# Optimization experiments

Hardware: AMD Instinct MI355X
Metric: run time of the kernel (lower is better)

The kernel has to match this reference:

```python
import jax, jax.numpy as jnp
import numpy as np
import math

NUM_ITER = 5
FEAT_STRIDE = 16
GAUSS_SIGMA = 1.0
HINGE_THRESHOLD = -999.0
MIN_FILTER_REG = 1e-3
ALPHA_EPS = 0.0


def apply_filter(feat, weights):
    # feat: (ni, ns, C, H, W); weights: (ns, C, fH, fW) -> scores (ni, ns, oH, oW)
    ni, ns, C, H, W = feat.shape
    fH, fW = weights.shape[-2], weights.shape[-1]
    x = feat.reshape(ni, ns * C, H, W)
    out = jax.lax.conv_general_dilated(
        x, weights, window_strides=(1, 1),
        padding=((fH // 2, fH // 2), (fW // 2, fW // 2)),
        dimension_numbers=('NCHW', 'OIHW', 'NCHW'),
        feature_group_count=ns)
    return out  # (ni, ns, oH, oW); oH = H + (fH+1)%2


def get_label(center, out_sz, sigma):
    # center: (ni, ns, 2) in (row, col) order
    k0 = jnp.arange(out_sz[0], dtype=jnp.float32)[None, None, :, None]
    k1 = jnp.arange(out_sz[1], dtype=jnp.float32)[None, None, None, :]
    g0 = jnp.exp(-0.5 / (sigma * sigma) * (k0 - center[..., 0][..., None, None]) ** 2)
    g1 = jnp.exp(-0.5 / (sigma * sigma) * (k1 - center[..., 1][..., None, None]) ** 2)
    return g0 * g1  # (ni, ns, oH, oW)


def _forward(weights, feat, bb, log_step_length, filter_reg):
    ni, ns = feat.shape[0], feat.shape[1]
    fH, fW = weights.shape[-2], weights.shape[-1]
    out_sz = (feat.shape[-2] + (fH + 1) % 2, feat.shape[-1] + (fW + 1) % 2)
    step = jnp.exp(log_step_length)[0]
    reg = jnp.maximum(filter_reg * filter_reg, MIN_FILTER_REG ** 2)[0]
    dmap_offset = jnp.array([fH % 2, fW % 2], jnp.float32) / 2.0
    # (x, y) -> (row, col), feature-grid coordinates
    center = ((bb[..., :2] + bb[..., 2:] / 2.0) / FEAT_STRIDE)[..., ::-1] - dmap_offset
    label = get_label(center, out_sz, GAUSS_SIGMA)
    mask = (label > HINGE_THRESHOLD).astype(feat.dtype)
    label = label * mask
    sw = math.sqrt(1.0 / ni)

    losses = []
    for _ in range(NUM_ITER):
        scores = apply_filter(feat, weights)
        scores_act = mask * scores + (1.0 - mask) * jax.nn.relu(scores)
        score_mask = mask + (1.0 - mask) * (jax.lax.stop_gradient(scores) > 0).astype(scores.dtype)
        residuals = sw * (scores_act - label)
        losses.append((jnp.sum(residuals ** 2) + reg * jnp.sum(weights ** 2)) / ns)
        residuals_mapped = score_mask * (sw * residuals)
        # feat-transpose = adjoint of apply_filter w.r.t. the filter weights
        _, vjp_fn = jax.vjp(lambda w: apply_filter(feat, w), weights)
        data_grad = vjp_fn(residuals_mapped)[0]
        weights_grad = data_grad + reg * weights
        scores_grad = apply_filter(feat, weights_grad)
        scores_grad = sw * (score_mask * scores_grad)
        alpha_num = jnp.sum(weights_grad ** 2, axis=(1, 2, 3))  # (ns,)
        alpha_den = jnp.maximum(
            jnp.sum(scores_grad.reshape(ni, ns, -1) ** 2, axis=(0, 2))
            + (reg + ALPHA_EPS) * alpha_num, 1e-8)
        alpha = alpha_num / alpha_den
        weights = weights - step * alpha[:, None, None, None] * weights_grad

    scores = apply_filter(feat, weights)
    scores = mask * scores + (1.0 - mask) * jax.nn.relu(scores)
    losses.append((jnp.sum((sw * (scores - label)) ** 2) + reg * jnp.sum(weights ** 2)) / ns)
    return weights, jnp.stack(losses)


def setup_inputs() -> dict:
    key = jax.random.key(0)
    k1, k2, k3, k4 = jax.random.split(key, 4)
    ni, ns, C, H, W, fH, fW = 3, 32, 512, 22, 22, 4, 4
    weights = 0.01 * jax.random.normal(k1, (ns, C, fH, fW), jnp.float32)
    feat = jax.random.normal(k2, (ni, ns, C, H, W), jnp.float32)
    # boxes (x, y, w, h) in image coords (image size = 22*16 = 352)
    xy = jax.random.uniform(k3, (ni, ns, 2), jnp.float32, 50.0, 250.0)
    wh = jax.random.uniform(k4, (ni, ns, 2), jnp.float32, 32.0, 96.0)
    bb = jnp.concatenate([xy, wh], axis=-1)
    log_step_length = jnp.zeros((1,), jnp.float32)  # log(1.0)
    filter_reg = 0.01 * jnp.ones((1,), jnp.float32)
    return {"weights": weights, "feat": feat, "bb": bb,
            "log_step_length": log_step_length, "filter_reg": filter_reg}


def reference(weights, feat, bb, log_step_length, filter_reg):
    return _forward(weights, feat, bb, log_step_length, filter_reg)
```

## Files before the change

kernel.cpp:

```cpp
#include <hip/hip_runtime.h>
#include <hip/hip_fp16.h>

#define NI 3
#define NS 32
#define CHN 512
#define OH 23
#define P2 529
#define NP 50784
#define UV 484
#define WSZ 262144
#define KTOT 1536
#define RSP 1544

typedef unsigned int uint32;
typedef unsigned short u16;
typedef _Float16 h2 __attribute__((ext_vector_type(2)));
typedef _Float16 f16x8 __attribute__((ext_vector_type(8)));
typedef float f32x4 __attribute__((ext_vector_type(4)));

#define OFF_FEATT 0UL
#define OFF_LABEL 47579136UL
#define OFF_S0    47782272UL
#define OFF_S1    47985408UL
#define OFF_SGRAW 48188544UL
#define OFF_WG    48391680UL
#define OFF_WGF16 49440256UL
#define OFF_W0F16 49964544UL
#define OFF_PART  50488832UL
#define OFF_FEATC 50521600UL
#define OFF_S0B   100853248UL
#define OFF_SGB   101056384UL

#define P_DEN   0
#define P_NUM   4320
#define P_LOSS  5600
#define P_WSQ0  5760
#define P_WSQA  5792
#define P_WSQ5  6816
#define P_L5    7840

__device__ __forceinline__ float waveSum(float v) {
#pragma unroll
  for (int o = 32; o > 0; o >>= 1) v += __shfl_xor(v, o, 64);
  return v;
}

__global__ __launch_bounds__(256) void k_setup(const float* __restrict__ feat,
                                               const float* __restrict__ w0,
                                               const float* __restrict__ bb,
                                               u16* __restrict__ featT,
                                               u16* __restrict__ featC,
                                               u16* __restrict__ w0f16,
                                               float* __restrict__ wmaster,
                                               float* __restrict__ label,
                                               float* __restrict__ part) {
  __shared__ uint32 lds32[64 * 121];
  __shared__ float sred[4];
  int b = blockIdx.x, tid = threadIdx.x;
  if (b < 1536) {
    int snT = b >> 4, r4 = b & 15;
    int cb = r4 >> 1, uvh = r4 & 1;
    int s = snT / 3, n = snT % 3;
    const float* fsrc =
        feat + ((size_t)n * NS + s) * CHN * UV + (size_t)(cb * 64) * UV + uvh * 242;
#pragma unroll
    for (int it = 0; it < 31; ++it) {
      int idx = it * 256 + tid;
      if (idx < 7744) {
        int r = (unsigned)idx / 121u;
        int j = idx - r * 121;
        float2 v = *(const float2*)(fsrc + (size_t)r * UV + 2 * j);
        lds32[idx] = (uint32)__half_as_ushort(__float2half(v.x)) |
                     ((uint32)__half_as_ushort(__float2half(v.y)) << 16);
      }
    }
    __syncthreads();
    uint32* dstT = (uint32*)featT +
                   ((size_t)(snT * 4 + (cb >> 1)) * UV + uvh * 242) * 64 + (cb & 1) * 32;
#pragma unroll
    for (int it = 0; it < 16; ++it) {
      int o = it * 256 + tid;
      if (o < 3872) {
        int uv = o >> 4, kp = o & 15;
        int j = uv >> 1, sh = (uv & 1) * 16;
        uint32 a0 = lds32[(4 * kp + 0) * 121 + j];
        uint32 a1 = lds32[(4 * kp + 1) * 121 + j];
        uint32 a2 = lds32[(4 * kp + 2) * 121 + j];
        uint32 a3 = lds32[(4 * kp + 3) * 121 + j];
        uint2 val;
        val.x = ((a0 >> sh) & 0xffffu) | (((a1 >> sh) & 0xffffu) << 16);
        val.y = ((a2 >> sh) & 0xffffu) | (((a3 >> sh) & 0xffffu) << 16);
        *(uint2*)(dstT + (size_t)uv * 64 + 2 * kp) = val;
      }
    }
    uint32* dstC =
        (uint32*)featC + ((size_t)(s * CHN + cb * 64)) * 768 + n * 256 + uvh * 121;
    if (uvh == 0) {
#pragma unroll
      for (int it = 0; it < 31; ++it) {
        int idx = it * 256 + tid;
        if (idx < 7744) {
          int c = (unsigned)idx / 121u;
          int j = idx - c * 121;
          dstC[(size_t)c * 768 + j] = lds32[idx];
        }
      }
    } else {
#pragma unroll
      for (int it = 0; it < 34; ++it) {
        int idx = it * 256 + tid;
        if (idx < 8640) {
          int c = (unsigned)idx / 135u;
          int j = idx - c * 135;
          dstC[(size_t)c * 768 + j] = (j < 121) ? lds32[c * 121 + j] : 0u;
        }
      }
    }
  } else if (b < 1568) {
    int s = b - 1536;
    for (int i = tid; i < 8192; i += 256) {
      int tap = i >> 9, c = i & 511;
      w0f16[(size_t)s * 8192 + i] =
          __half_as_ushort(__float2half(w0[(size_t)s * 8192 + c * 16 + tap]));
    }
    float sq = 0.f;
    for (int i = tid; i < 8192; i += 256) {
      float v = w0[(size_t)s * 8192 + i];
      wmaster[(size_t)s * 8192 + i] = v;
      sq += v * v;
    }
    sq = waveSum(sq);
    if ((tid & 63) == 0) sred[tid >> 6] = sq;
    __syncthreads();
    if (tid == 0) part[P_WSQ0 + s] = sred[0] + sred[1] + sred[2] + sred[3];
  } else {
    int p = (b - 1568) * 256 + tid;
    if (p < NP) {
      int nsid = p / P2, rem = p % P2;
      int i = rem / OH, j = rem % OH;
      const float* bp = bb + (size_t)nsid * 4;
      float cr = (bp[1] + 0.5f * bp[3]) * 0.0625f;
      float cc = (bp[0] + 0.5f * bp[2]) * 0.0625f;
      float dy = (float)i - cr, dx = (float)j - cc;
      label[p] = __expf(-0.5f * (dy * dy + dx * dx));
    }
  }
}

__global__ __launch_bounds__(1024) void k_conv_fwd(const u16* __restrict__ featT,
                                                   const u16* __restrict__ wf16,
                                                   float* __restrict__ outA,
                                                   float* __restrict__ outB) {
  __shared__ uint32 w_lds[16 * 132];
  __shared__ float G[496 * 17];
  int tid = threadIdx.x;
  int bidx = blockIdx.x;
  int snT = bidx >> 1, ch = bidx & 1;
  int s = snT / 3, n = snT - s * 3;
  const uint32* wsrc = (const uint32*)(wf16 + (size_t)s * 8192) + ch * 128;
  for (int i = tid; i < 2048; i += 1024) {
    int tap = i >> 7, p = i & 127;
    w_lds[tap * 132 + p] = wsrc[(size_t)tap * 256 + p];
  }
  __syncthreads();
  int wave = tid >> 6, lane = tid & 63;
  int q = lane >> 4, m16 = lane & 15;
  int t0 = wave, t1 = wave + 16;
  bool has2 = (t1 < 31);
  f32x4 acc0 = {0.f, 0.f, 0.f, 0.f}, acc1 = {0.f, 0.f, 0.f, 0.f};
  size_t base = (size_t)snT * 4 * UV * 128;
  int r0i = t0 * 16 + m16;
  int r1i = has2 ? t1 * 16 + m16 : 483;
  if (r1i > 483) r1i = 483;
  size_t row0 = (size_t)r0i * 128;
  size_t row1 = (size_t)r1i * 128;
#pragma unroll
  for (int ks = 0; ks < 8; ++ks) {
    int cb = ch * 2 + (ks >> 2), cin = (ks & 3) * 32;
    size_t cbase = base + (size_t)cb * UV * 128 + cin + q * 8;
    f16x8 a0 = *(const f16x8*)(featT + cbase + row0);
    uint4 bw = *(const uint4*)&w_lds[m16 * 132 + ks * 16 + q * 4];
    f16x8 bf = __builtin_bit_cast(f16x8, bw);
    acc0 = __builtin_amdgcn_mfma_f32_16x16x32_f16(a0, bf, acc0, 0, 0, 0);
    if (has2) {
      f16x8 a1 = *(const f16x8*)(featT + cbase + row1);
      acc1 = __builtin_amdgcn_mfma_f32_16x16x32_f16(a1, bf, acc1, 0, 0, 0);
    }
  }
#pragma unroll
  for (int r = 0; r < 4; ++r) G[(t0 * 16 + q * 4 + r) * 17 + m16] = acc0[r];
  if (has2) {
#pragma unroll
    for (int r = 0; r < 4; ++r) G[(t1 * 16 + q * 4 + r) * 17 + m16] = acc1[r];
  }
  __syncthreads();
  if (tid < P2) {
    int y = tid / 23, x = tid - y * 23;
    float val = 0.f;
#pragma unroll
    for (int ky = 0; ky < 4; ++ky) {
      int u = y + ky - 2;
      if ((unsigned)u < 22u) {
#pragma unroll
        for (int kx = 0; kx < 4; ++kx) {
          int v = x + kx - 2;
          if ((unsigned)v < 22u) val += G[(u * 22 + v) * 17 + ky * 4 + kx];
        }
      }
    }
    float* dst = ch ? outB : outA;
    dst[(size_t)(n * NS + s) * P2 + tid] = val;
  }
}

__global__ __launch_bounds__(1024) void k_adjoint(
    int t, const u16* __restrict__ featC, const float* __restrict__ label,
    const float* __restrict__ s0a, const float* __restrict__ s0b,
    const float* __restrict__ scores_old, float* __restrict__ scores_new,
    const float* __restrict__ sga, const float* __restrict__ sgb,
    float* __restrict__ wg, u16* __restrict__ wgf16, float* __restrict__ wmaster,
    float* __restrict__ part, const float* __restrict__ lsl,
    const float* __restrict__ fr) {
  __shared__ float r_lds[3 * P2];
  __shared__ __align__(16) u16 rs[16 * RSP];
  __shared__ __align__(16) float kred[3 * 4 * 64 * 4];
  __shared__ float lred[16], nred[16], wred[16], dend[16];
  int tid = threadIdx.x;
  int s = blockIdx.x >> 3, chunk = blockIdx.x & 7;
  int c0 = chunk * 64;
  float step = __expf(lsl[0]);
  float frv = fr[0];
  float reg = fmaxf(frv * frv, 1e-6f);

  float alpha_p = 0.f;
  if (t >= 1) {
    const float* np_ = part + P_NUM + (size_t)((t - 1) * NS + s) * 8;
    float nu = 0.f;
#pragma unroll
    for (int i = 0; i < 8; ++i) nu += np_[i];
    float dp = 0.f;
    for (int pl = tid; pl < 1587; pl += 1024) {
      int nn = (unsigned)pl / (unsigned)P2;
      int rem = pl - nn * P2;
      size_t gp = (size_t)(nn * NS + s) * P2 + rem;
      float g = sga[gp] + sgb[gp];
      dp += g * g;
    }
    dp = waveSum(dp);
    if ((tid & 63) == 0) dend[tid >> 6] = dp;
    __syncthreads();
    float de = 0.f;
#pragma unroll
    for (int i = 0; i < 16; ++i) de += dend[i];
    alpha_p = nu / fmaxf(de * (1.0f / 3.0f) + reg * nu, 1e-8f);
  }

  float lsum = 0.f;
  for (int pl = tid; pl < 1587; pl += 1024) {
    int nn = (unsigned)pl / (unsigned)P2;
    int rem = pl - nn * P2;
    size_t gp = (size_t)(nn * NS + s) * P2 + rem;
    float S = (t <= 1) ? (s0a[gp] + s0b[gp]) : scores_old[gp];
    if (t >= 1) S -= step * alpha_p * (sga[gp] + sgb[gp]);
    float d = S - label[gp];
    r_lds[nn * P2 + rem] = d * (1.0f / 3.0f);
    if (chunk == 0) {
      if (t >= 1) scores_new[gp] = S;
      lsum += d * d;
    }
  }
  lsum = waveSum(lsum);
  if ((tid & 63) == 0) lred[tid >> 6] = lsum;
  __syncthreads();
  if (chunk == 0 && tid == 0) {
    float L = 0.f;
#pragma unroll
    for (int i = 0; i < 16; ++i) L += lred[i];
    part[P_LOSS + t * NS + s] = L * (1.0f / 3.0f);
  }

  for (int idx = tid; idx < 16 * RSP; idx += 1024) {
    int tap = (unsigned)idx / (unsigned)RSP;
    int k = idx - tap * RSP;
    float val = 0.f;
    if (k < KTOT) {
      int n = k >> 9, uv = k & 511;
      if (uv < UV) {
        int u = (unsigned)uv / 22u;
        int v = uv - u * 22;
        int ky = tap >> 2, kx = tap & 3;
        int y = u + 2 - ky, x = v + 2 - kx;
        if ((unsigned)y < 23u && (unsigned)x < 23u) val = r_lds[n * P2 + y * OH + x];
      }
    }
    rs[idx] = __half_as_ushort(__float2half(val));
  }
  __syncthreads();

  int wave = tid >> 6, lane = tid & 63;
  int q = lane >> 4, m16 = lane & 15;
  int tile = wave & 3, kq = wave >> 2;
  int c = c0 + tile * 16 + m16;
  const u16* arow = featC + ((size_t)(s * CHN + c)) * KTOT + kq * 384 + q * 8;
  const u16* brow = rs + m16 * RSP + kq * 384 + q * 8;
  f32x4 acc = {0.f, 0.f, 0.f, 0.f};
#pragma unroll
  for (int ks = 0; ks < 12; ++ks) {
    f16x8 a = *(const f16x8*)(arow + ks * 32);
    f16x8 bf = *(const f16x8*)(brow + ks * 32);
    acc = __builtin_amdgcn_mfma_f32_16x16x32_f16(a, bf, acc, 0, 0, 0);
  }
  if (kq) *(f32x4*)&kred[(((kq - 1) * 4 + tile) * 64 + lane) * 4] = acc;
  __syncthreads();

  float num_part = 0.f, wsq_part = 0.f;
  if (kq == 0) {
#pragma unroll
    for (int kk = 0; kk < 3; ++kk)
      acc += *(const f32x4*)&kred[((kk * 4 + tile) * 64 + lane) * 4];
    int tap = m16;
    int ccb = c0 + tile * 16 + q * 4;
    union { u16 h[4]; uint2 v2; } pk;
#pragma unroll
    for (int r = 0; r < 4; ++r) {
      int cc = ccb + r;
      size_t widx = (size_t)s * 8192 + (size_t)cc * 16 + tap;
      float wold = wmaster[widx];
      float wnew = wold;
      if (t >= 1) {
        wnew = wold - step * alpha_p * wg[widx];
        wmaster[widx] = wnew;
      }
      float wgn = acc[r] + reg * wnew;
      wg[widx] = wgn;
      pk.h[r] = __half_as_ushort(__float2half(wgn));
      wsq_part += wnew * wnew;
      num_part += wgn * wgn;
    }
    *(uint2*)&wgf16[(size_t)s * 8192 + (size_t)tap * 512 + ccb] = pk.v2;
  }
  num_part = waveSum(num_part);
  wsq_part = waveSum(wsq_part);
  if (lane == 0) {
    nred[wave] = num_part;
    wred[wave] = wsq_part;
  }
  __syncthreads();
  if (tid == 0) {
    float nsum = 0.f, wsum = 0.f;
#pragma unroll
    for (int i = 0; i < 16; ++i) {
      nsum += nred[i];
      wsum += wred[i];
    }
    part[P_NUM + (size_t)(t * NS + s) * 8 + chunk] = nsum;
    if (t >= 1) part[P_WSQA + (size_t)((t - 1) * NS + s) * 8 + chunk] = wsum;
  }
}

__global__ __launch_bounds__(1024) void k_den(const float* __restrict__ sga,
                                              const float* __restrict__ sgb,
                                              float* __restrict__ part) {
  __shared__ float dend[16];
  int s = blockIdx.x, tid = threadIdx.x;
  float dp = 0.f;
  for (int pl = tid; pl < 1587; pl += 1024) {
    int nn = (unsigned)pl / (unsigned)P2;
    int rem = pl - nn * P2;
    size_t gp = (size_t)(nn * NS + s) * P2 + rem;
    float g = sga[gp] + sgb[gp];
    dp += g * g;
  }
  dp = waveSum(dp);
  if ((tid & 63) == 0) dend[tid >> 6] = dp;
  __syncthreads();
  if (tid == 0) {
    float de = 0.f;
#pragma unroll
    for (int i = 0; i < 16; ++i) de += dend[i];
    part[P_DEN + s] = de * (1.0f / 3.0f);
  }
}

__device__ __forceinline__ float alphaFinal(const float* __restrict__ part, int s,
                                            float reg) {
  const float* np_ = part + P_NUM + (size_t)(4 * NS + s) * 8;
  float nu = 0.f;
#pragma unroll
  for (int i = 0; i < 8; ++i) nu += np_[i];
  float de = part[P_DEN + s];
  return nu / fmaxf(de + reg * nu, 1e-8f);
}

__global__ void k_final(float* __restrict__ wmaster, const float* __restrict__ wg,
                        const float* __restrict__ scores4, const float* __restrict__ sga,
                        const float* __restrict__ sgb, const float* __restrict__ label,
                        float* __restrict__ part, const float* __restrict__ lsl,
                        const float* __restrict__ fr) {
  __shared__ float alpha_s[32];
  __shared__ float red4[4];
  int b = blockIdx.x, tid = threadIdx.x;
  float step = __expf(lsl[0]);
  float frv = fr[0];
  float reg = fmaxf(frv * frv, 1e-6f);
  if (tid < 32) alpha_s[tid] = alphaFinal(part, tid, reg);
  __syncthreads();
  if (b < 1024) {
    int idx = b * 256 + tid;
    int s = idx >> 13;
    float w5 = wmaster[idx] - step * alpha_s[s] * wg[idx];
    wmaster[idx] = w5;
    float sq = waveSum(w5 * w5);
    if ((tid & 63) == 0) red4[tid >> 6] = sq;
    __syncthreads();
    if (tid == 0) part[P_WSQ5 + b] = red4[0] + red4[1] + red4[2] + red4[3];
  } else {
    int p = (b - 1024) * 256 + tid;
    float contrib = 0.f;
    if (p < NP) {
      int nsid = p / P2;
      int s = nsid & 31;
      float s5 = scores4[p] - step * alpha_s[s] * (sga[p] + sgb[p]);
      float d = s5 - label[p];
      contrib = d * d;
    }
    contrib = waveSum(contrib);
    if ((tid & 63) == 0) red4[tid >> 6] = contrib;
    __syncthreads();
    if (tid == 0)
      part[P_L5 + (b - 1024)] = (red4[0] + red4[1] + red4[2] + red4[3]) * (1.0f / 3.0f);
  }
}

__global__ void k_losses(float* __restrict__ out_losses, const float* __restrict__ part,
                         const float* __restrict__ fr) {
  __shared__ float red[8];
  int tid = threadIdx.x;
  float frv = fr[0];
  float reg = fmaxf(frv * frv, 1e-6f);
  float v5 = 0.f;
  for (int i = tid; i < 1024; i += 256) v5 += part[P_WSQ5 + i];
  v5 = waveSum(v5);
  if ((tid & 63) == 0) red[tid >> 6] = v5;
  __syncthreads();
  float wsq5 = red[0] + red[1] + red[2] + red[3];
  float l5 = 0.f;
  for (int i = tid; i < 199; i += 256) l5 += part[P_L5 + i];
  l5 = waveSum(l5);
  if ((tid & 63) == 0) red[4 + (tid >> 6)] = l5;
  __syncthreads();
  float loss5 = red[4] + red[5] + red[6] + red[7];
  if (tid < 5) {
    int t = tid;
    float ls = 0.f;
    for (int i = 0; i < 32; ++i) ls += part[P_LOSS + t * NS + i];
    float ws_ = 0.f;
    if (t == 0) {
      for (int i = 0; i < 32; ++i) ws_ += part[P_WSQ0 + i];
    } else {
      for (int i = 0; i < 256; ++i) ws_ += part[P_WSQA + (t - 1) * 256 + i];
    }
    out_losses[t] = (ls + reg * ws_) * (1.0f / 32.0f);
  }
  if (tid == 5) out_losses[5] = (loss5 + reg * wsq5) * (1.0f / 32.0f);
}

extern "C" void kernel_launch(void* const* d_in, const int* in_sizes, int n_in,
                              void* d_out, int out_size, void* d_ws, size_t ws_size,
                              hipStream_t stream) {
  const float* w0 = (const float*)d_in[0];
  const float* feat = (const float*)d_in[1];
  const float* bb = (const float*)d_in[2];
  const float* lsl = (const float*)d_in[3];
  const float* fr = (const float*)d_in[4];
  float* out = (float*)d_out;
  char* ws = (char*)d_ws;
  u16* featT = (u16*)(ws + OFF_FEATT);
  float* label = (float*)(ws + OFF_LABEL);
  float* s0 = (float*)(ws + OFF_S0);
  float* s0b = (float*)(ws + OFF_S0B);
  float* s1 = (float*)(ws + OFF_S1);
  float* sga = (float*)(ws + OFF_SGRAW);
  float* sgb = (float*)(ws + OFF_SGB);
  float* wg = (float*)(ws + OFF_WG);
  u16* wgf16 = (u16*)(ws + OFF_WGF16);
  u16* w0f16 = (u16*)(ws + OFF_W0F16);
  float* part = (float*)(ws + OFF_PART);
  u16* featC = (u16*)(ws + OFF_FEATC);

  k_setup<<<1767, 256, 0, stream>>>(feat, w0, bb, featT, featC, w0f16, out, label, part);
  k_conv_fwd<<<192, 1024, 0, stream>>>(featT, w0f16, s0, s0b);
  for (int t = 0; t < 5; ++t) {
    const float* so = (t <= 1) ? s0 : ((t & 1) ? s0 : s1);
    float* sn = (t & 1) ? s1 : s0;
    k_adjoint<<<256, 1024, 0, stream>>>(t, featC, label, s0, s0b, so, sn, sga, sgb, wg,
                                        wgf16, out, part, lsl, fr);
    k_conv_fwd<<<192, 1024, 0, stream>>>(featT, wgf16, sga, sgb);
  }
  k_den<<<32, 1024, 0, stream>>>(sga, sgb, part);
  k_final<<<1223, 256, 0, stream>>>(out, wg, s0, sga, sgb, label, part, lsl, fr);
  k_losses<<<1, 256, 0, stream>>>(out + WSZ, part, fr);
}
```

Before: 358.9 us.

## Build channel-major feature copy lazily inside first adjoint pass with k-blocked layout

Removes the featC transpose/write from the setup kernel. The first adjoint iteration now reads fp32 features directly, converts them to fp16, feeds them to the MFMA and writes them out in a new k-block-major layout. Later iterations read that layout with strided loads. This saves one pass over the features in setup and overlaps the conversion with compute, but the first adjoint becomes heavier and reads from global memory with less coalescing.

```diff
diff --git a/kernel.cpp b/kernel.cpp
--- a/kernel.cpp
+++ b/kernel.cpp
@@ -10,6 +10,7 @@
 #define UV 484
 #define WSZ 262144
 #define KTOT 1536
+#define NKB 48
 #define RSP 1544
 
 typedef unsigned int uint32;
@@ -49,7 +50,6 @@
                                                const float* __restrict__ w0,
                                                const float* __restrict__ bb,
                                                u16* __restrict__ featT,
-                                               u16* __restrict__ featC,
                                                u16* __restrict__ w0f16,
                                                float* __restrict__ wmaster,
                                                float* __restrict__ label,
@@ -93,29 +93,6 @@
         *(uint2*)(dstT + (size_t)uv * 64 + 2 * kp) = val;
       }
     }
-    uint32* dstC =
-        (uint32*)featC + ((size_t)(s * CHN + cb * 64)) * 768 + n * 256 + uvh * 121;
-    if (uvh == 0) {
-#pragma unroll
-      for (int it = 0; it < 31; ++it) {
-        int idx = it * 256 + tid;
-        if (idx < 7744) {
-          int c = (unsigned)idx / 121u;
-          int j = idx - c * 121;
-          dstC[(size_t)c * 768 + j] = lds32[idx];
-        }
-      }
-    } else {
-#pragma unroll
-      for (int it = 0; it < 34; ++it) {
-        int idx = it * 256 + tid;
-        if (idx < 8640) {
-          int c = (unsigned)idx / 135u;
-          int j = idx - c * 135;
-          dstC[(size_t)c * 768 + j] = (j < 121) ? lds32[c * 121 + j] : 0u;
-        }
-      }
-    }
   } else if (b < 1568) {
     int s = b - 1536;
     for (int i = tid; i < 8192; i += 256) {
@@ -214,12 +191,12 @@
 }
 
 __global__ __launch_bounds__(1024) void k_adjoint(
-    int t, const u16* __restrict__ featC, const float* __restrict__ label,
-    const float* __restrict__ s0a, const float* __restrict__ s0b,
-    const float* __restrict__ scores_old, float* __restrict__ scores_new,
-    const float* __restrict__ sga, const float* __restrict__ sgb,
-    float* __restrict__ wg, u16* __restrict__ wgf16, float* __restrict__ wmaster,
-    float* __restrict__ part, const float* __restrict__ lsl,
+    int t, const float* __restrict__ feat, u16* __restrict__ featC,
+    const float* __restrict__ label, const float* __restrict__ s0a,
+    const float* __restrict__ s0b, const float* __restrict__ scores_old,
+    float* __restrict__ scores_new, const float* __restrict__ sga,
+    const float* __restrict__ sgb, float* __restrict__ wg, u16* __restrict__ wgf16,
+    float* __restrict__ wmaster, float* __restrict__ part, const float* __restrict__ lsl,
     const float* __restrict__ fr) {
   __shared__ float r_lds[3 * P2];
   __shared__ __align__(16) u16 rs[16 * RSP];
@@ -301,14 +278,44 @@
   int q = lane >> 4, m16 = lane & 15;
   int tile = wave & 3, kq = wave >> 2;
   int c = c0 + tile * 16 + m16;
-  const u16* arow = featC + ((size_t)(s * CHN + c)) * KTOT + kq * 384 + q * 8;
   const u16* brow = rs + m16 * RSP + kq * 384 + q * 8;
   f32x4 acc = {0.f, 0.f, 0.f, 0.f};
-#pragma unroll
-  for (int ks = 0; ks < 12; ++ks) {
-    f16x8 a = *(const f16x8*)(arow + ks * 32);
-    f16x8 bf = *(const f16x8*)(brow + ks * 32);
-    acc = __builtin_amdgcn_mfma_f32_16x16x32_f16(a, bf, acc, 0, 0, 0);
+  if (t == 0) {
+#pragma unroll
+    for (int ks = 0; ks < 12; ++ks) {
+      int kb = kq * 12 + ks;
+      int k0 = kb * 32 + q * 8;
+      int nn = k0 >> 9, uv0 = k0 & 511;
+      float v[8];
+#pragma unroll
+      for (int i = 0; i < 8; ++i) v[i] = 0.f;
+      if (uv0 < UV) {
+        const float* fsrc = feat + ((size_t)(nn * NS + s) * CHN + c) * UV + uv0;
+        if (uv0 + 8 <= UV) {
+          float4 p0 = *(const float4*)fsrc;
+          float4 p1 = *(const float4*)(fsrc + 4);
+          v[0] = p0.x; v[1] = p0.y; v[2] = p0.z; v[3] = p0.w;
+          v[4] = p1.x; v[5] = p1.y; v[6] = p1.z; v[7] = p1.w;
+        } else {
+#pragma unroll
+          for (int i = 0; i < 4; ++i) v[i] = fsrc[i];
+        }
+      }
+      union { u16 h[8]; f16x8 f; uint4 u; } av;
+#pragma unroll
+      for (int i = 0; i < 8; ++i) av.h[i] = __half_as_ushort(__float2half(v[i]));
+      *(uint4*)(featC + (((size_t)(s * NKB + kb) * CHN + c) * 32 + q * 8)) = av.u;
+      f16x8 bf = *(const f16x8*)(brow + ks * 32);
+      acc = __builtin_amdgcn_mfma_f32_16x16x32_f16(av.f, bf, acc, 0, 0, 0);
+    }
+  } else {
+    const u16* arow = featC + ((size_t)(s * NKB + kq * 12) * CHN + c) * 32 + q * 8;
+#pragma unroll
+    for (int ks = 0; ks < 12; ++ks) {
+      f16x8 a = *(const f16x8*)(arow + (size_t)ks * (CHN * 32));
+      f16x8 bf = *(const f16x8*)(brow + ks * 32);
+      acc = __builtin_amdgcn_mfma_f32_16x16x32_f16(a, bf, acc, 0, 0, 0);
+    }
   }
   if (kq) *(f32x4*)&kred[(((kq - 1) * 4 + tile) * 64 + lane) * 4] = acc;
   __syncthreads();
@@ -488,13 +495,13 @@
   float* part = (float*)(ws + OFF_PART);
   u16* featC = (u16*)(ws + OFF_FEATC);
 
-  k_setup<<<1767, 256, 0, stream>>>(feat, w0, bb, featT, featC, w0f16, out, label, part);
+  k_setup<<<1767, 256, 0, stream>>>(feat, w0, bb, featT, w0f16, out, label, part);
   k_conv_fwd<<<192, 1024, 0, stream>>>(featT, w0f16, s0, s0b);
   for (int t = 0; t < 5; ++t) {
     const float* so = (t <= 1) ? s0 : ((t & 1) ? s0 : s1);
     float* sn = (t & 1) ? s1 : s0;
-    k_adjoint<<<256, 1024, 0, stream>>>(t, featC, label, s0, s0b, so, sn, sga, sgb, wg,
-                                        wgf16, out, part, lsl, fr);
+    k_adjoint<<<256, 1024, 0, stream>>>(t, feat, featC, label, s0, s0b, so, sn, sga, sgb,
+                                        wg, wgf16, out, part, lsl, fr);
     k_conv_fwd<<<192, 1024, 0, stream>>>(featT, wgf16, sga, sgb);
   }
   k_den<<<32, 1024, 0, stream>>>(sga, sgb, part);
```

New measurement: 356.1 us. No clear change (-0.8%).
